# Performance work log

Measured on AMD Instinct MI355X. Metric: run time of the kernel, lower is better.

The kernel has to match this reference:

```python
import jax, jax.numpy as jnp
import numpy as np

# Model config (matches init_kwargs)
HIDDEN = 2048
N_HEADS = 32
N_KV_HEADS = 8
HEAD_DIM = 64
BS = 8  # block_size_x = block_size_y = block_size_z


def setup_inputs() -> dict:
    key = jax.random.key(0)
    ks = jax.random.split(key, 5)
    B, X, Y, Z = 2, 16, 16, 16
    L = X * Y * Z  # 4096
    s = 1.0 / np.sqrt(HIDDEN)
    return {
        "hidden_states": jax.random.normal(ks[0], (B, L, HIDDEN), jnp.float32),
        "Wq": jax.random.normal(ks[1], (N_HEADS * HEAD_DIM, HIDDEN), jnp.float32) * s,
        "Wk": jax.random.normal(ks[2], (N_KV_HEADS * HEAD_DIM, HIDDEN), jnp.float32) * s,
        "Wv": jax.random.normal(ks[3], (N_KV_HEADS * HEAD_DIM, HIDDEN), jnp.float32) * s,
        "Wo": jax.random.normal(ks[4], (HIDDEN, N_HEADS * HEAD_DIM), jnp.float32) * s,
        "x_dim": 16,
        "y_dim": 16,
        "z_dim": 16,
    }


def _to_blocks(t, B, x_dim, y_dim, z_dim, H):
    # t: [B, L, H*D] with L interpreted as (x, y, z) row-major grid.
    # einops: 'b (bnx bsx bny bsy bnz bsz) (h d) -> (b bnx bny bnz) (bsx bsy bsz) h d'
    bnx, bny, bnz = x_dim // BS, y_dim // BS, z_dim // BS
    t = t.reshape(B, bnx, BS, bny, BS, bnz, BS, H, HEAD_DIM)
    t = t.transpose(0, 1, 3, 5, 2, 4, 6, 7, 8)  # [B,bnx,bny,bnz,bsx,bsy,bsz,H,D]
    return t.reshape(B * bnx * bny * bnz, BS * BS * BS, H, HEAD_DIM)


def _from_blocks(o, B, x_dim, y_dim, z_dim):
    bnx, bny, bnz = x_dim // BS, y_dim // BS, z_dim // BS
    o = o.reshape(B, bnx, bny, bnz, BS, BS, BS, N_HEADS, HEAD_DIM)
    o = o.transpose(0, 1, 4, 2, 5, 3, 6, 7, 8)  # back to (bnx bsx bny bsy bnz bsz)
    return o.reshape(B, x_dim * y_dim * z_dim, N_HEADS * HEAD_DIM)


def reference(hidden_states, Wq, Wk, Wv, Wo, x_dim, y_dim, z_dim):
    B, L, _ = hidden_states.shape
    q = _to_blocks(hidden_states @ Wq.T, B, x_dim, y_dim, z_dim, N_HEADS)     # [NB,T,H,D]
    k = _to_blocks(hidden_states @ Wk.T, B, x_dim, y_dim, z_dim, N_KV_HEADS)  # [NB,T,Hk,D]
    v = _to_blocks(hidden_states @ Wv.T, B, x_dim, y_dim, z_dim, N_KV_HEADS)
    # GQA: repeat kv heads across groups (flash_attn handles this internally)
    g = N_HEADS // N_KV_HEADS
    k = jnp.repeat(k, g, axis=2)
    v = jnp.repeat(v, g, axis=2)
    scale = HEAD_DIM ** -0.5
    # non-causal full attention within each 3D block
    scores = jnp.einsum('bthd,bshd->bhts', q, k) * scale  # [NB,H,T,T]
    p = jax.nn.softmax(scores, axis=-1)
    o = jnp.einsum('bhts,bshd->bthd', p, v)               # [NB,T,H,D]
    o = _from_blocks(o, B, x_dim, y_dim, z_dim)           # [B,L,H*D]
    return o @ Wo.T
```

## Files before the change

kernel.cpp:

```cpp
#include <hip/hip_runtime.h>

typedef _Float16 f16;
typedef _Float16 f16x4 __attribute__((ext_vector_type(4)));
typedef _Float16 f16x8 __attribute__((ext_vector_type(8)));
typedef float f32x4 __attribute__((ext_vector_type(4)));
typedef unsigned int u32;
typedef u32 u32x4 __attribute__((ext_vector_type(4)));

__device__ __forceinline__ f32x4 mfma16(f16x8 a, f16x8 b, f32x4 c) {
  return __builtin_amdgcn_mfma_f32_16x16x32_f16(a, b, c, 0, 0, 0);
}

__device__ __forceinline__ void gld_lds16(const void* g, void* l) {
  __builtin_amdgcn_global_load_lds(
      (const __attribute__((address_space(1))) void*)g,
      (__attribute__((address_space(3))) void*)l, 16, 0, 0);
}

__device__ __forceinline__ u32 pkrtz(float a, float b) {
  return __builtin_bit_cast(u32, __builtin_amdgcn_cvt_pkrtz(a, b));
}

#define XSWZ(row) (((row) & 7) << 4)

__global__ __launch_bounds__(256) void cast5_k(
    const float4* s0, const float4* s1, const float4* s2, const float4* s3,
    const float4* s4, f16x4* d0, f16x4* d1, f16x4* d2, f16x4* d3, f16x4* d4,
    int e0, int e1, int e2, int e3, int e4) {
  int i = blockIdx.x * blockDim.x + threadIdx.x;
  int stride = gridDim.x * blockDim.x;
  for (; i < e4; i += stride) {
    const float4* s = s0; f16x4* d = d0; int base = 0;
    if (i >= e0) { s = s1; d = d1; base = e0; }
    if (i >= e1) { s = s2; d = d2; base = e1; }
    if (i >= e2) { s = s3; d = d3; base = e2; }
    if (i >= e3) { s = s4; d = d4; base = e3; }
    float4 v = s[i - base];
    f16x4 o;
    o.x = (f16)v.x; o.y = (f16)v.y; o.z = (f16)v.z; o.w = (f16)v.w;
    d[i - base] = o;
  }
}

template <typename OutT>
__global__ __launch_bounds__(256, 2) void gemm_bt(
    const f16* __restrict__ A, const f16* __restrict__ B, OutT* __restrict__ C,
    int M, int N, int K, float oscale) {
  __shared__ __align__(16) f16 Al[128 * 64];
  __shared__ __align__(16) f16 Bl[128 * 64];
  const int tid = threadIdx.x;
  const int lane = tid & 63;
  const int wave = tid >> 6;
  const int bm = blockIdx.x, bn = blockIdx.y;
  const int wm = wave >> 1, wn = wave & 1;
  f32x4 acc[4][4] = {};

  const size_t ldb = (size_t)K * 2;
  const char* Ab = (const char*)A + (size_t)bm * 128 * ldb;
  const char* Bb = (const char*)B + (size_t)bn * 128 * ldb;

  const int kTiles = K >> 6;
  for (int kt = 0; kt < kTiles; ++kt) {
    const size_t kOff = (size_t)kt << 7;
    __syncthreads();
#pragma unroll
    for (int i = 0; i < 4; ++i) {
      int c = i * 256 + tid;
      int row = c >> 3;
      int colb = ((c & 7) << 4) ^ XSWZ(row);
      gld_lds16(Ab + (size_t)row * ldb + kOff + colb,
                (char*)Al + (i * 256 + wave * 64) * 16);
      gld_lds16(Bb + (size_t)row * ldb + kOff + colb,
                (char*)Bl + (i * 256 + wave * 64) * 16);
    }
    __syncthreads();
#pragma unroll
    for (int kk = 0; kk < 2; ++kk) {
      const int kb = kk * 64 + ((lane >> 4) << 4);
      f16x8 af[4], bf[4];
#pragma unroll
      for (int mf = 0; mf < 4; ++mf) {
        int row = wm * 64 + mf * 16 + (lane & 15);
        af[mf] = *(const f16x8*)((const char*)Al + (row << 7) + (kb ^ XSWZ(row)));
      }
#pragma unroll
      for (int nf = 0; nf < 4; ++nf) {
        int row = wn * 64 + nf * 16 + (lane & 15);
        bf[nf] = *(const f16x8*)((const char*)Bl + (row << 7) + (kb ^ XSWZ(row)));
      }
#pragma unroll
      for (int mf = 0; mf < 4; ++mf)
#pragma unroll
        for (int nf = 0; nf < 4; ++nf)
          acc[mf][nf] = mfma16(af[mf], bf[nf], acc[mf][nf]);
    }
  }
  const int r0 = ((lane >> 4) << 2);
  const int cl = lane & 15;
#pragma unroll
  for (int mf = 0; mf < 4; ++mf)
#pragma unroll
    for (int r = 0; r < 4; ++r) {
      size_t row = (size_t)bm * 128 + wm * 64 + mf * 16 + r0 + r;
#pragma unroll
      for (int nf = 0; nf < 4; ++nf) {
        int col = bn * 128 + wn * 64 + nf * 16 + cl;
        C[row * N + col] = (OutT)(acc[mf][nf][r] * oscale);
      }
    }
}

template <typename OutT>
__global__ __launch_bounds__(512, 2) void gemm_bt8(
    const f16* __restrict__ A, const f16* __restrict__ B, OutT* __restrict__ C,
    int M, int N, int K, float oscale) {
  __shared__ __align__(16) char lds[131072];
  const int tid = threadIdx.x;
  const int lane = tid & 63;
  const int wave = tid >> 6;
  const int wm = wave >> 2, wn = wave & 3;
  const int l15 = lane & 15, g = lane >> 4;
  const int bid = blockIdx.x;
  const int bm = (bid & 7) * 4 + ((bid >> 3) & 3);
  const int bn = bid >> 5;

  const size_t ldb = (size_t)K * 2;
  const int r0 = tid >> 2, r1 = 128 + (tid >> 2);
  const int chx = (((tid & 3) ^ ((tid >> 3) & 3)) << 4);
  const char* As0 = (const char*)A + (size_t)(bm * 256 + r0) * ldb + chx;
  const char* As1 = (const char*)A + (size_t)(bm * 256 + r1) * ldb + chx;
  const char* Bs0 = (const char*)B + (size_t)(bn * 256 + r0) * ldb + chx;
  const char* Bs1 = (const char*)B + (size_t)(bn * 256 + r1) * ldb + chx;

  auto stA = [&](int buf, int t, int kh) {
    char* dst = (char*)lds + (buf * 2 + kh) * 16384 + wave * 1024;
    size_t ko = (size_t)t * 128 + (size_t)kh * 64;
    gld_lds16(As0 + ko, dst);
    gld_lds16(As1 + ko, dst + 8192);
  };
  auto stB = [&](int buf, int t, int kh) {
    char* dst = (char*)lds + 65536 + (buf * 2 + kh) * 16384 + wave * 1024;
    size_t ko = (size_t)t * 128 + (size_t)kh * 64;
    gld_lds16(Bs0 + ko, dst);
    gld_lds16(Bs1 + ko, dst + 8192);
  };

  int aoff[8], boff[4];
  const int rsw = (g ^ ((l15 >> 1) & 3)) << 4;
#pragma unroll
  for (int mf = 0; mf < 8; ++mf)
    aoff[mf] = (wm * 128 + mf * 16 + l15) * 64 + rsw;
#pragma unroll
  for (int nf = 0; nf < 4; ++nf)
    boff[nf] = (wn * 64 + nf * 16 + l15) * 64 + rsw;

  f32x4 acc[8][4] = {};

  stA(0, 0, 0); stB(0, 0, 0); stA(0, 0, 1); stB(0, 0, 1);
  stA(1, 1, 0); stB(1, 1, 0); stA(1, 1, 1);
  asm volatile("s_waitcnt vmcnt(6)" ::: "memory");
  __builtin_amdgcn_s_barrier();

  const int nkt = K >> 6;
  for (int T = 0; T < nkt; ++T) {
    const int cur = T & 1;
    const char* A0 = (const char*)lds + (cur * 2 + 0) * 16384;
    const char* A1 = (const char*)lds + (cur * 2 + 1) * 16384;
    const char* B0r = (const char*)lds + 65536 + (cur * 2 + 0) * 16384;
    const char* B1r = (const char*)lds + 65536 + (cur * 2 + 1) * 16384;
    f16x8 a[8], b0, b1;
#pragma unroll
    for (int mf = 0; mf < 8; ++mf) a[mf] = *(const f16x8*)(A0 + aoff[mf]);
    b0 = *(const f16x8*)(B0r + boff[0]);
    b1 = *(const f16x8*)(B0r + boff[1]);
    if (T + 1 < nkt) stB(cur ^ 1, T + 1, 1);
    __builtin_amdgcn_s_barrier();
    __builtin_amdgcn_s_setprio(1);
#pragma unroll
    for (int mf = 0; mf < 8; ++mf) {
      acc[mf][0] = mfma16(a[mf], b0, acc[mf][0]);
      acc[mf][1] = mfma16(a[mf], b1, acc[mf][1]);
    }
    __builtin_amdgcn_s_setprio(0);
    __builtin_amdgcn_s_barrier();
    b0 = *(const f16x8*)(B0r + boff[2]);
    b1 = *(const f16x8*)(B0r + boff[3]);
    if (T + 2 < nkt) stA(cur, T + 2, 0);
    __builtin_amdgcn_s_barrier();
    __builtin_amdgcn_s_setprio(1);
#pragma unroll
    for (int mf = 0; mf < 8; ++mf) {
      acc[mf][2] = mfma16(a[mf], b0, acc[mf][2]);
      acc[mf][3] = mfma16(a[mf], b1, acc[mf][3]);
    }
    __builtin_amdgcn_s_setprio(0);
    __builtin_amdgcn_s_barrier();
#pragma unroll
    for (int mf = 0; mf < 8; ++mf) a[mf] = *(const f16x8*)(A1 + aoff[mf]);
    b0 = *(const f16x8*)(B1r + boff[0]);
    b1 = *(const f16x8*)(B1r + boff[1]);
    if (T + 2 < nkt) stB(cur, T + 2, 0);
    __builtin_amdgcn_s_barrier();
    __builtin_amdgcn_s_setprio(1);
#pragma unroll
    for (int mf = 0; mf < 8; ++mf) {
      acc[mf][0] = mfma16(a[mf], b0, acc[mf][0]);
      acc[mf][1] = mfma16(a[mf], b1, acc[mf][1]);
    }
    __builtin_amdgcn_s_setprio(0);
    __builtin_amdgcn_s_barrier();
    b0 = *(const f16x8*)(B1r + boff[2]);
    b1 = *(const f16x8*)(B1r + boff[3]);
    if (T + 2 < nkt) stA(cur, T + 2, 1);
    if (T < nkt - 2) asm volatile("s_waitcnt vmcnt(6)" ::: "memory");
    else             asm volatile("s_waitcnt vmcnt(0)" ::: "memory");
    __builtin_amdgcn_s_barrier();
    __builtin_amdgcn_s_setprio(1);
#pragma unroll
    for (int mf = 0; mf < 8; ++mf) {
      acc[mf][2] = mfma16(a[mf], b0, acc[mf][2]);
      acc[mf][3] = mfma16(a[mf], b1, acc[mf][3]);
    }
    __builtin_amdgcn_s_setprio(0);
    __builtin_amdgcn_s_barrier();
  }
#pragma unroll
  for (int mf = 0; mf < 8; ++mf)
#pragma unroll
    for (int r = 0; r < 4; ++r) {
      size_t row = (size_t)bm * 256 + wm * 128 + mf * 16 + g * 4 + r;
#pragma unroll
      for (int nf = 0; nf < 4; ++nf) {
        int col = bn * 256 + wn * 64 + nf * 16 + l15;
        C[row * (size_t)N + col] = (OutT)(acc[mf][nf][r] * oscale);
      }
    }
}

__device__ __forceinline__ int tok_row(int nb, int t) {
  int b = nb >> 3;
  int x = (((nb >> 2) & 1) << 3) | (t >> 6);
  int y = (((nb >> 1) & 1) << 3) | ((t >> 3) & 7);
  int z = ((nb & 1) << 3) | (t & 7);
  return (b << 12) | (x << 8) | (y << 4) | z;
}

__global__ __launch_bounds__(512, 4) void attn3d(
    const f16* __restrict__ Q, const f16* __restrict__ KV, f16* __restrict__ O) {
  __shared__ __align__(16) f16 Kl[2][64 * 64];
  __shared__ __align__(16) f16 Vt[2][64 * 64];
  const int tid = threadIdx.x;
  const int lane = tid & 63;
  const int wave = tid >> 6;
  const int fid = blockIdx.x;
  const int orig = (fid & 7) * 128 + (fid >> 3);
  const int qt = orig & 1, h = (orig >> 1) & 31, nb = orig >> 6;
  const int hk = h >> 2;
  const int l15 = lane & 15;
  const int g = lane >> 4;
  const size_t ldkv = 2048;

  const int pos2 = (((lane & 3) | (((lane >> 4) & 1) << 2) |
                     (((lane >> 2) & 3) << 3) | ((lane >> 5) << 5))) * 2;

  const int krow = tid >> 3;
  const int kcolb = ((tid & 7) << 4) ^ XSWZ(krow);

  f16x8 bq[2][2];
#pragma unroll
  for (int qf = 0; qf < 2; ++qf) {
    const char* qrow = (const char*)Q +
        (size_t)tok_row(nb, qt * 256 + wave * 32 + qf * 16 + l15) * 4096 + h * 128;
#pragma unroll
    for (int kk = 0; kk < 2; ++kk)
      bq[qf][kk] = *(const f16x8*)(qrow + kk * 64 + g * 16);
  }

  {
    gld_lds16((const char*)KV + (size_t)tok_row(nb, krow) * ldkv + hk * 128 + kcolb,
              (char*)Kl[0] + wave * 1024);
    f16x8 vch = *(const f16x8*)((const char*)KV +
        (size_t)tok_row(nb, lane) * ldkv + 1024 + hk * 128 + wave * 16);
    asm volatile("s_waitcnt vmcnt(0)" ::: "memory");
    const int dbase = wave * 8;
#pragma unroll
    for (int j = 0; j < 8; ++j)
      *(f16*)((char*)Vt[0] + ((dbase + j) << 7) + (pos2 ^ (j << 4))) = vch[j];
    __syncthreads();
  }

  f32x4 o[2][4] = {};
  float lacc[2] = {0.f, 0.f};

  for (int kt = 0; kt < 8; ++kt) {
    const int b = kt & 1;
    const char* Kb = (const char*)Kl[b];
    const char* Vb = (const char*)Vt[b];
    f16x8 vch;
    if (kt < 7) {
      gld_lds16((const char*)KV + (size_t)tok_row(nb, (kt + 1) * 64 + krow) * ldkv + hk * 128 + kcolb,
                (char*)Kl[b ^ 1] + wave * 1024);
      vch = *(const f16x8*)((const char*)KV +
          (size_t)tok_row(nb, (kt + 1) * 64 + lane) * ldkv + 1024 + hk * 128 + wave * 16);
    }
    f32x4 s[2][4] = {};
    __builtin_amdgcn_s_setprio(1);
#pragma unroll
    for (int kk = 0; kk < 2; ++kk) {
      const int kb = kk * 64 + (g << 4);
      f16x8 ka[4];
#pragma unroll
      for (int nf = 0; nf < 4; ++nf) {
        int kr = nf * 16 + l15;
        ka[nf] = *(const f16x8*)(Kb + (kr << 7) + (kb ^ XSWZ(kr)));
      }
#pragma unroll
      for (int qf = 0; qf < 2; ++qf)
#pragma unroll
        for (int nf = 0; nf < 4; ++nf)
          s[qf][nf] = mfma16(ka[nf], bq[qf][kk], s[qf][nf]);
    }
    __builtin_amdgcn_s_setprio(0);
#pragma unroll
    for (int qf = 0; qf < 2; ++qf) {
      float ls = 0.f;
#pragma unroll
      for (int nf = 0; nf < 4; ++nf)
#pragma unroll
        for (int r = 0; r < 4; ++r) {
          float p = __builtin_amdgcn_exp2f(s[qf][nf][r]);
          s[qf][nf][r] = p;
          ls += p;
        }
      lacc[qf] += ls;
    }
    __builtin_amdgcn_s_setprio(1);
#pragma unroll
    for (int kh = 0; kh < 2; ++kh) {
      f16x8 va[4];
      const int cb = kh * 64 + g * 16;
#pragma unroll
      for (int df = 0; df < 4; ++df) {
        int d = df * 16 + l15;
        va[df] = *(const f16x8*)(Vb + (d << 7) + (cb ^ XSWZ(d)));
      }
#pragma unroll
      for (int qf = 0; qf < 2; ++qf) {
        u32x4 pw = {pkrtz(s[qf][2 * kh][0], s[qf][2 * kh][1]),
                    pkrtz(s[qf][2 * kh][2], s[qf][2 * kh][3]),
                    pkrtz(s[qf][2 * kh + 1][0], s[qf][2 * kh + 1][1]),
                    pkrtz(s[qf][2 * kh + 1][2], s[qf][2 * kh + 1][3])};
        f16x8 pfh = __builtin_bit_cast(f16x8, pw);
#pragma unroll
        for (int df = 0; df < 4; ++df)
          o[qf][df] = mfma16(va[df], pfh, o[qf][df]);
      }
    }
    __builtin_amdgcn_s_setprio(0);
    if (kt < 7) {
      asm volatile("s_waitcnt vmcnt(0)" ::: "memory");
      const int dbase = wave * 8;
#pragma unroll
      for (int j = 0; j < 8; ++j)
        *(f16*)((char*)Vt[b ^ 1] + ((dbase + j) << 7) + (pos2 ^ (j << 4))) = vch[j];
      __syncthreads();
    }
  }
#pragma unroll
  for (int qf = 0; qf < 2; ++qf) {
    float l = lacc[qf];
    l += __shfl_xor(l, 16);
    l += __shfl_xor(l, 32);
    float inv = 1.f / l;
    int t = qt * 256 + wave * 32 + qf * 16 + l15;
    char* dst = (char*)O + (size_t)tok_row(nb, t) * 4096 + h * 128;
#pragma unroll
    for (int df = 0; df < 4; ++df) {
      f16x4 o4;
#pragma unroll
      for (int r = 0; r < 4; ++r) o4[r] = (f16)(o[qf][df][r] * inv);
      *(f16x4*)(dst + df * 32 + g * 8) = o4;
    }
  }
}

extern "C" void kernel_launch(void* const* d_in, const int* in_sizes, int n_in,
                              void* d_out, int out_size, void* d_ws, size_t ws_size,
                              hipStream_t stream) {
  (void)in_sizes; (void)n_in; (void)out_size; (void)ws_size;
  const float* hs = (const float*)d_in[0];
  const float* Wq = (const float*)d_in[1];
  const float* Wk = (const float*)d_in[2];
  const float* Wv = (const float*)d_in[3];
  const float* Wo = (const float*)d_in[4];
  float* out = (float*)d_out;
  char* ws = (char*)d_ws;

  f16* hid16 = (f16*)(ws + 0);
  f16* Wq16  = (f16*)(ws + 33554432);
  f16* Wk16  = (f16*)(ws + 41943040);
  f16* Wv16  = (f16*)(ws + 44040192);
  f16* Wo16  = (f16*)(ws + 46137344);
  f16* Q16   = (f16*)(ws + 54525952);
  f16* KV16  = (f16*)(ws + 88080384);

  cast5_k<<<2048, 256, 0, stream>>>(
      (const float4*)hs, (const float4*)Wq, (const float4*)Wk,
      (const float4*)Wv, (const float4*)Wo,
      (f16x4*)hid16, (f16x4*)Wq16, (f16x4*)Wk16, (f16x4*)Wv16, (f16x4*)Wo16,
      4194304, 5242880, 5505024, 5767168, 6815744);

  gemm_bt8<f16><<<256, 512, 0, stream>>>(hid16, Wq16, Q16, 8192, 2048, 2048,
                                         0.18033688011112042f);
  gemm_bt<f16><<<dim3(64, 8), 256, 0, stream>>>(hid16, Wk16, KV16, 8192, 1024, 2048, 1.0f);

  attn3d<<<1024, 512, 0, stream>>>(Q16, KV16, hid16);

  gemm_bt8<float><<<256, 512, 0, stream>>>(hid16, Wo16, out, 8192, 2048, 2048, 1.0f);
}
```

Baseline: 268.1 us.

## Use quadrant-pipelined GEMM variant for output projection

```diff
diff --git a/kernel.cpp b/kernel.cpp
--- a/kernel.cpp
+++ b/kernel.cpp
@@ -237,6 +237,164 @@
     }
 }
 
+template <typename OutT>
+__global__ __launch_bounds__(512, 1) void gemm_bt8q(
+    const f16* __restrict__ A, const f16* __restrict__ B, OutT* __restrict__ C,
+    int M, int N, int K, float oscale) {
+  __shared__ __align__(16) char lds[131072];
+  const int tid = threadIdx.x;
+  const int lane = tid & 63;
+  const int wave = tid >> 6;
+  const int wm = wave >> 2, wn = wave & 3;
+  const int l15 = lane & 15, g = lane >> 4;
+  const int bid = blockIdx.x;
+  const int bm = (bid & 7) * 4 + ((bid >> 3) & 3);
+  const int bn = bid >> 5;
+
+  const size_t ldb = (size_t)K * 2;
+  const int chq = (((tid & 7) ^ ((tid >> 3) & 7)) << 4);
+  const int srow = tid >> 3;
+
+  auto stage = [&](const f16* X, int rowbase, char* region, int t) {
+#pragma unroll
+    for (int it = 0; it < 2; ++it) {
+      const char* src = (const char*)X +
+          (size_t)(rowbase + it * 64 + srow) * ldb + (size_t)t * 128 + chq;
+      gld_lds16(src, region + (it * 512 + wave * 64) * 16);
+    }
+  };
+  auto Areg = [&](int buf, int mh) { return (char*)lds + (buf * 2 + mh) * 16384; };
+  auto Breg = [&](int buf, int mh) { return (char*)lds + 65536 + (buf * 2 + mh) * 16384; };
+
+  int aoff[8][2], boff[4][2];
+#pragma unroll
+  for (int mf = 0; mf < 8; ++mf) {
+    int row = mf * 16 + l15;
+#pragma unroll
+    for (int kk = 0; kk < 2; ++kk)
+      aoff[mf][kk] = (row << 7) + ((kk * 64 + g * 16) ^ XSWZ(row));
+  }
+#pragma unroll
+  for (int nf = 0; nf < 4; ++nf) {
+    int row = (wn & 1) * 64 + nf * 16 + l15;
+#pragma unroll
+    for (int kk = 0; kk < 2; ++kk)
+      boff[nf][kk] = (row << 7) + ((kk * 64 + g * 16) ^ XSWZ(row));
+  }
+
+  f32x4 acc[8][4] = {};
+
+  stage(A, bm * 256 + 0,   Areg(0, 0), 0);
+  stage(A, bm * 256 + 128, Areg(0, 1), 0);
+  stage(B, bn * 256 + 0,   Breg(0, 0), 0);
+  stage(B, bn * 256 + 128, Breg(0, 1), 0);
+  stage(A, bm * 256 + 0,   Areg(1, 0), 1);
+  stage(A, bm * 256 + 128, Areg(1, 1), 1);
+  asm volatile("s_waitcnt vmcnt(4)" ::: "memory");
+  __builtin_amdgcn_s_barrier();
+
+  const int nkt = K >> 6;
+  for (int T = 0; T < nkt; ++T) {
+    const int b = T & 1;
+    const char* Aw = Areg(b, wm);
+    const char* Bw = Breg(b, wn >> 1);
+    f16x8 a[4][2], bf[2][2];
+#pragma unroll
+    for (int mf = 0; mf < 4; ++mf)
+#pragma unroll
+      for (int kk = 0; kk < 2; ++kk)
+        a[mf][kk] = *(const f16x8*)(Aw + aoff[mf][kk]);
+#pragma unroll
+    for (int nf = 0; nf < 2; ++nf)
+#pragma unroll
+      for (int kk = 0; kk < 2; ++kk)
+        bf[nf][kk] = *(const f16x8*)(Bw + boff[nf][kk]);
+    if (T + 1 < nkt) stage(B, bn * 256 + 0, Breg(b ^ 1, 0), T + 1);
+    __builtin_amdgcn_s_barrier();
+    __builtin_amdgcn_s_setprio(1);
+#pragma unroll
+    for (int mf = 0; mf < 4; ++mf)
+#pragma unroll
+      for (int nf = 0; nf < 2; ++nf) {
+        acc[mf][nf] = mfma16(a[mf][0], bf[nf][0], acc[mf][nf]);
+        acc[mf][nf] = mfma16(a[mf][1], bf[nf][1], acc[mf][nf]);
+      }
+    __builtin_amdgcn_s_setprio(0);
+    __builtin_amdgcn_s_barrier();
+#pragma unroll
+    for (int nf = 0; nf < 2; ++nf)
+#pragma unroll
+      for (int kk = 0; kk < 2; ++kk)
+        bf[nf][kk] = *(const f16x8*)(Bw + boff[2 + nf][kk]);
+    if (T + 1 < nkt) stage(B, bn * 256 + 128, Breg(b ^ 1, 1), T + 1);
+    __builtin_amdgcn_s_barrier();
+    __builtin_amdgcn_s_setprio(1);
+#pragma unroll
+    for (int mf = 0; mf < 4; ++mf)
+#pragma unroll
+      for (int nf = 0; nf < 2; ++nf) {
+        acc[mf][2 + nf] = mfma16(a[mf][0], bf[nf][0], acc[mf][2 + nf]);
+        acc[mf][2 + nf] = mfma16(a[mf][1], bf[nf][1], acc[mf][2 + nf]);
+      }
+    __builtin_amdgcn_s_setprio(0);
+    __builtin_amdgcn_s_barrier();
+#pragma unroll
+    for (int mf = 0; mf < 4; ++mf)
+#pragma unroll
+      for (int kk = 0; kk < 2; ++kk)
+        a[mf][kk] = *(const f16x8*)(Aw + aoff[4 + mf][kk]);
+#pragma unroll
+    for (int nf = 0; nf < 2; ++nf)
+#pragma unroll
+      for (int kk = 0; kk < 2; ++kk)
+        bf[nf][kk] = *(const f16x8*)(Bw + boff[nf][kk]);
+    __builtin_amdgcn_s_barrier();
+    __builtin_amdgcn_s_setprio(1);
+#pragma unroll
+    for (int mf = 0; mf < 4; ++mf)
+#pragma unroll
+      for (int nf = 0; nf < 2; ++nf) {
+        acc[4 + mf][nf] = mfma16(a[mf][0], bf[nf][0], acc[4 + mf][nf]);
+        acc[4 + mf][nf] = mfma16(a[mf][1], bf[nf][1], acc[4 + mf][nf]);
+      }
+    __builtin_amdgcn_s_setprio(0);
+    __builtin_amdgcn_s_barrier();
+#pragma unroll
+    for (int nf = 0; nf < 2; ++nf)
+#pragma unroll
+      for (int kk = 0; kk < 2; ++kk)
+        bf[nf][kk] = *(const f16x8*)(Bw + boff[2 + nf][kk]);
+    if (T + 2 < nkt) {
+      stage(A, bm * 256 + 0,   Areg(b, 0), T + 2);
+      stage(A, bm * 256 + 128, Areg(b, 1), T + 2);
+    }
+    if (T < nkt - 2) asm volatile("s_waitcnt vmcnt(4)" ::: "memory");
+    else             asm volatile("s_waitcnt vmcnt(0)" ::: "memory");
+    __builtin_amdgcn_s_barrier();
+    __builtin_amdgcn_s_setprio(1);
+#pragma unroll
+    for (int mf = 0; mf < 4; ++mf)
+#pragma unroll
+      for (int nf = 0; nf < 2; ++nf) {
+        acc[4 + mf][2 + nf] = mfma16(a[mf][0], bf[nf][0], acc[4 + mf][2 + nf]);
+        acc[4 + mf][2 + nf] = mfma16(a[mf][1], bf[nf][1], acc[4 + mf][2 + nf]);
+      }
+    __builtin_amdgcn_s_setprio(0);
+    __builtin_amdgcn_s_barrier();
+  }
+#pragma unroll
+  for (int mf = 0; mf < 8; ++mf)
+#pragma unroll
+    for (int r = 0; r < 4; ++r) {
+      size_t row = (size_t)bm * 256 + wm * 128 + mf * 16 + g * 4 + r;
+#pragma unroll
+      for (int nf = 0; nf < 4; ++nf) {
+        int col = bn * 256 + wn * 64 + nf * 16 + l15;
+        C[row * (size_t)N + col] = (OutT)(acc[mf][nf][r] * oscale);
+      }
+    }
+}
+
 __device__ __forceinline__ int tok_row(int nb, int t) {
   int b = nb >> 3;
   int x = (((nb >> 2) & 1) << 3) | (t >> 6);
@@ -416,5 +574,5 @@
 
   attn3d<<<1024, 512, 0, stream>>>(Q16, KV16, hid16);
 
-  gemm_bt8<float><<<256, 512, 0, stream>>>(hid16, Wo16, out, 8192, 2048, 2048, 1.0f);
-}
+  gemm_bt8q<float><<<256, 512, 0, stream>>>(hid16, Wo16, out, 8192, 2048, 2048, 1.0f);
+}
```

Result: no change. 268.6 us (+0.2%).
